# Optimization experiments

Hardware: AMD Instinct MI355X
Metric: run time of the kernel (lower is better)

Reference implementation:

```python
import jax, jax.numpy as jnp
import numpy as np

N_NODES = 65536
N_EDGES = 1048576
D = 128           # input_dim == hidden_dim*heads, residual active everywhere
HEADS = (4, 4, 1) # heads per GATv2 layer; last layer heads=1, out=input_dim
NUM_LAYERS = 3


def setup_inputs() -> dict:
    key = jax.random.key(0)
    ks = jax.random.split(key, 16)
    x = jax.random.normal(ks[0], (N_NODES, D), dtype=jnp.float32)
    edge_src = jax.random.randint(ks[1], (N_EDGES,), 0, N_NODES)
    edge_dst = jax.random.randint(ks[2], (N_EDGES,), 0, N_NODES)
    edge_attr = jax.random.uniform(ks[3], (N_EDGES, 1), dtype=jnp.float32)
    s = 0.05
    Wl = jax.random.normal(ks[4], (NUM_LAYERS, D, D), dtype=jnp.float32) * s
    bl = jnp.zeros((NUM_LAYERS, D), dtype=jnp.float32)
    Wr = jax.random.normal(ks[5], (NUM_LAYERS, D, D), dtype=jnp.float32) * s
    br = jnp.zeros((NUM_LAYERS, D), dtype=jnp.float32)
    We = jax.random.normal(ks[6], (NUM_LAYERS, 1, D), dtype=jnp.float32) * s
    att = jax.random.normal(ks[7], (NUM_LAYERS, D), dtype=jnp.float32) * s  # reshaped (H,C) per layer
    bias_p = jnp.zeros((NUM_LAYERS, D), dtype=jnp.float32)
    ln_g = jnp.ones((NUM_LAYERS, D), dtype=jnp.float32)
    ln_b = jnp.zeros((NUM_LAYERS, D), dtype=jnp.float32)
    return {"x": x, "edge_src": edge_src, "edge_dst": edge_dst, "edge_attr": edge_attr,
            "Wl": Wl, "bl": bl, "Wr": Wr, "br": br, "We": We, "att": att,
            "bias_p": bias_p, "ln_g": ln_g, "ln_b": ln_b, "num_graphs": 128}


def _layer_norm(x, g, b):
    mu = x.mean(-1, keepdims=True)
    var = jnp.mean((x - mu) ** 2, axis=-1, keepdims=True)
    return (x - mu) * jax.lax.rsqrt(var + 1e-5) * g + b


def _gatv2(x, src, dst, ea, Wl, bl, Wr, br, We, att, bias, H):
    # GATv2Conv, eval mode (no dropout), concat heads
    N = x.shape[0]
    HC = Wl.shape[1]
    C = HC // H
    xl = (x @ Wl + bl).reshape(N, H, C)
    xr = (x @ Wr + br).reshape(N, H, C)
    ee = (ea @ We).reshape(-1, H, C)            # [E, H, C]
    m = xl[src] + xr[dst] + ee                  # gather + fuse edge features
    m = jnp.where(m >= 0, m, 0.2 * m)           # leaky_relu(0.2)
    a = jnp.einsum('ehc,hc->eh', m, att.reshape(H, C))
    # scatter-softmax over destination node neighborhoods
    amax = jax.ops.segment_max(a, dst, num_segments=N)
    ae = jnp.exp(a - amax[dst])
    asum = jax.ops.segment_sum(ae, dst, num_segments=N)
    alpha = ae / (asum[dst] + 1e-16)
    out = jax.ops.segment_sum(xl[src] * alpha[:, :, None], dst, num_segments=N)
    return out.reshape(N, HC) + bias


def reference(x, edge_src, edge_dst, edge_attr, Wl, bl, Wr, br, We, att,
              bias_p, ln_g, ln_b, num_graphs):
    N = x.shape[0]
    # add_self_loops=True with fill_value='mean' for edge_attr (PyG default)
    loop = jnp.arange(N, dtype=edge_src.dtype)
    src = jnp.concatenate([edge_src, loop])
    dst = jnp.concatenate([edge_dst, loop])
    ea_mean = edge_attr.mean(0, keepdims=True)
    ea = jnp.concatenate([edge_attr, jnp.broadcast_to(ea_mean, (N, edge_attr.shape[1]))])
    h = x
    for i in range(NUM_LAYERS):
        out = _gatv2(h, src, dst, ea, Wl[i], bl[i], Wr[i], br[i], We[i],
                     att[i], bias_p[i], HEADS[i])
        out = _layer_norm(out, ln_g[i], ln_b[i])
        if i < NUM_LAYERS - 1:
            out = jax.nn.gelu(out, approximate=False)
        h = h + out  # residual: dims match at every layer by construction
    # to_dense_batch with equal-size graphs, then drop virtual node (last per graph)
    x_dense = h.reshape(num_graphs, -1, h.shape[-1])
    return x_dense[:, :-1, :]
```

## Files before the change

kernel.cpp:

```cpp
#include <hip/hip_runtime.h>
#include <hip/hip_bf16.h>

typedef unsigned int uint;
typedef unsigned short ushort;

#define NN 65536
#define NE 1048576
#define DD 128
#define TOTE (NE + NN)

__device__ __forceinline__ float b2f(ushort u) {
    uint v = ((uint)u) << 16; float f; __builtin_memcpy(&f, &v, 4); return f;
}
__device__ __forceinline__ ushort f2b(float f) {
    uint x; __builtin_memcpy(&x, &f, 4);
    uint r = (x + 0x7fffu + ((x >> 16) & 1u)) >> 16;
    return (ushort)r;
}

typedef __bf16 bf16x8 __attribute__((ext_vector_type(8)));
typedef float f32x4 __attribute__((ext_vector_type(4)));
typedef float f32x2 __attribute__((ext_vector_type(2)));

__device__ __forceinline__ f32x2 bf2f2(uint u) {
    union { uint i; float f; } lo, hi;
    lo.i = u << 16; hi.i = u & 0xffff0000u;
    return (f32x2){lo.f, hi.f};
}


__global__ void k_init(const float* __restrict__ Wl, const float* __restrict__ Wr,
                       ushort* __restrict__ WT, int* __restrict__ cnt, float* __restrict__ sumbuf,
                       float* __restrict__ cano) {
    if (cano && blockIdx.x == 0 && blockIdx.y == 0 && blockIdx.z == 0 && threadIdx.x == 0)
        cano[0] = 100.0f;
    int k = blockIdx.x, n = threadIdx.x, lr = blockIdx.y, layer = blockIdx.z;
    const float* W = (lr ? Wr : Wl) + layer * 16384;
    WT[(layer * 2 + lr) * 16384 + n * 128 + k] = f2b(W[k * 128 + n]);
    int gid = ((blockIdx.z * 2 + blockIdx.y) * 128 + blockIdx.x) * 128 + threadIdx.x;
    if (gid < NN) cnt[gid] = 0;
    if (gid == NN) sumbuf[0] = 0.f;
}

__global__ void k_histsum(const int* __restrict__ dst, const float* __restrict__ ea,
                          int* __restrict__ cnt, float* __restrict__ sum,
                          float* __restrict__ cano) {
    if (cano && blockIdx.x == 0 && threadIdx.x == 0) cano[1] = 120.0f;
    __shared__ float red[256];
    int t = threadIdx.x;
    int e = blockIdx.x * 256 + t;
    int d = (e < NE) ? dst[e] : (e - NE);
    atomicAdd(&cnt[d], 1);
    float s = (e < NE) ? ea[e] : 0.f;
    red[t] = s; __syncthreads();
    for (int o = 128; o > 0; o >>= 1) { if (t < o) red[t] += red[t + o]; __syncthreads(); }
    if (t == 0 && red[0] != 0.f) atomicAdd(sum, red[0]);
}

__global__ void k_scanA(const int* __restrict__ cnt, int* __restrict__ row_off, int* __restrict__ bsum,
                        float* __restrict__ cano) {
    if (cano && blockIdx.x == 0 && threadIdx.x == 0) cano[2] = 140.0f;
    __shared__ int tmp[256];
    int t = threadIdx.x, i = blockIdx.x * 256 + t;
    int v = cnt[i]; tmp[t] = v; __syncthreads();
    for (int off = 1; off < 256; off <<= 1) {
        int x = (t >= off) ? tmp[t - off] : 0;
        __syncthreads();
        tmp[t] += x;
        __syncthreads();
    }
    row_off[i] = tmp[t] - v;
    if (t == 255) bsum[blockIdx.x] = tmp[255];
}

__global__ void k_scanC(int* __restrict__ row_off, const int* __restrict__ bsum, int* __restrict__ cursor,
                        float* __restrict__ cano) {
    if (cano && blockIdx.x == 0 && threadIdx.x == 0) cano[3] = 160.0f;
    __shared__ int tmp[256];
    __shared__ int excl[256];
    int t = threadIdx.x;
    int v = bsum[t]; tmp[t] = v; __syncthreads();
    for (int off = 1; off < 256; off <<= 1) {
        int x = (t >= off) ? tmp[t - off] : 0;
        __syncthreads();
        tmp[t] += x;
        __syncthreads();
    }
    excl[t] = tmp[t] - v;
    __syncthreads();
    int offb = excl[blockIdx.x];
    int i = blockIdx.x * 256 + t;
    int nv = row_off[i] + offb;
    row_off[i] = nv;
    cursor[i] = nv;
    if (i == 0) row_off[NN] = TOTE;
}

__global__ void k_scatter(const int* __restrict__ src, const int* __restrict__ dst,
                          const float* __restrict__ ea, const float* __restrict__ sum,
                          int* __restrict__ cursor, int2* __restrict__ adj,
                          float* __restrict__ cano) {
    if (cano && blockIdx.x == 0 && threadIdx.x == 0) cano[4] = 180.0f;
    int e = blockIdx.x * 256 + threadIdx.x;
    int s, d; float a;
    if (e < NE) { s = src[e]; d = dst[e]; a = ea[e]; }
    else        { s = e - NE; d = s;      a = sum[0] * (1.0f / NE); }
    int pos = atomicAdd(&cursor[d], 1);
    adj[pos] = make_int2(s << 8, __float_as_int(a));
}

#define LDA 136

template<bool F32SRC>
__global__ __launch_bounds__(256) void k_gemm(const void* __restrict__ srcv, const ushort* __restrict__ WT,
                                              const float* __restrict__ bl, const float* __restrict__ br,
                                              ushort* __restrict__ xl, ushort* __restrict__ xr,
                                              float* __restrict__ cano, int cslot, float cval) {
    if (cano && blockIdx.x == 0 && threadIdx.x == 0) cano[cslot] = cval;
    __shared__ ushort A[64 * LDA];
    int t = threadIdx.x;
    int rowbase = blockIdx.x * 64;

    if (F32SRC) {
        const float* src = (const float*)srcv;
        #pragma unroll
        for (int it = 0; it < 8; it++) {
            int idx = it * 256 + t;
            int r = idx >> 5, cc = (idx & 31) * 4;
            float4 v = *(const float4*)&src[(size_t)(rowbase + r) * 128 + cc];
            ushort4 pk; pk.x = f2b(v.x); pk.y = f2b(v.y); pk.z = f2b(v.z); pk.w = f2b(v.w);
            *(ushort4*)&A[r * LDA + cc] = pk;
        }
    } else {
        const ushort* src = (const ushort*)srcv;
        #pragma unroll
        for (int it = 0; it < 4; it++) {
            int idx = it * 256 + t;
            int r = idx >> 4, cc = (idx & 15) * 8;
            *(bf16x8*)&A[r * LDA + cc] = *(const bf16x8*)&src[(size_t)(rowbase + r) * 128 + cc];
        }
    }
    __syncthreads();

    int wave = t >> 6, lane = t & 63;
    int row16 = lane & 15, quad = lane >> 4;

    f32x4 accl[8], accr[8];
    for (int i = 0; i < 8; i++) {
        accl[i] = (f32x4){0.f, 0.f, 0.f, 0.f};
        accr[i] = (f32x4){0.f, 0.f, 0.f, 0.f};
    }

    for (int ks = 0; ks < 4; ks++) {
        bf16x8 a = *(const bf16x8*)&A[(wave * 16 + row16) * LDA + ks * 32 + quad * 8];
        for (int tc = 0; tc < 8; tc++) {
            int coln = tc * 16 + row16;
            bf16x8 b_l = *(const bf16x8*)&WT[coln * 128 + ks * 32 + quad * 8];
            bf16x8 b_r = *(const bf16x8*)&WT[16384 + coln * 128 + ks * 32 + quad * 8];
            accl[tc] = __builtin_amdgcn_mfma_f32_16x16x32_bf16(a, b_l, accl[tc], 0, 0, 0);
            accr[tc] = __builtin_amdgcn_mfma_f32_16x16x32_bf16(a, b_r, accr[tc], 0, 0, 0);
        }
    }

    for (int tc = 0; tc < 8; tc++) {
        int col = tc * 16 + row16;
        float bbl = bl[col], bbr = br[col];
        for (int r = 0; r < 4; r++) {
            int row = rowbase + wave * 16 + quad * 4 + r;
            size_t o = (size_t)row * 128 + col;
            xl[o] = f2b(accl[tc][r] + bbl);
            xr[o] = f2b(accr[tc][r] + bbr);
        }
    }
}

template<int H, bool FINAL>
__global__ __launch_bounds__(128, 4) void k_attn(
    const ushort* __restrict__ xl, const ushort* __restrict__ xr,
    const int* __restrict__ row_off, const int2* __restrict__ adj,
    const float* __restrict__ We, const float* __restrict__ att,
    const float* __restrict__ bias, const float* __restrict__ ln_g, const float* __restrict__ ln_b,
    const float* __restrict__ hin, float* __restrict__ hout, ushort* __restrict__ hb,
    float* __restrict__ outp,
    float* __restrict__ cano, int cslot, float cval)
{
    if (cano && blockIdx.x == 0 && threadIdx.x == 0) cano[cslot] = cval;
    __shared__ float accbuf[2][8][160];

    int wv = threadIdx.x >> 6, lane = threadIdx.x & 63;
    int n = blockIdx.x * 2 + wv;
    int p = lane >> 3;
    int cl = lane & 7;
    int c16 = cl * 16;
    const char* xlb = (const char*)xl;

    f32x2 we2[8], at2[8], xrl2[8];
    #pragma unroll
    for (int k = 0; k < 8; k++) {
        we2[k] = (f32x2){We[c16 + 2 * k], We[c16 + 2 * k + 1]};
        at2[k] = (f32x2){att[c16 + 2 * k], att[c16 + 2 * k + 1]};
    }
    {
        uint4 r0 = *(const uint4*)&xr[(size_t)n * 128 + c16];
        uint4 r1 = *(const uint4*)&xr[(size_t)n * 128 + c16 + 8];
        xrl2[0] = bf2f2(r0.x); xrl2[1] = bf2f2(r0.y); xrl2[2] = bf2f2(r0.z); xrl2[3] = bf2f2(r0.w);
        xrl2[4] = bf2f2(r1.x); xrl2[5] = bf2f2(r1.y); xrl2[6] = bf2f2(r1.z); xrl2[7] = bf2f2(r1.w);
    }

    int s0 = row_off[n], s1 = row_off[n + 1];
    int iters = (s1 - s0 + 7) >> 3;

    float l_run = 0.f;
    f32x2 acc[8];
    #pragma unroll
    for (int k = 0; k < 8; k++) acc[k] = (f32x2){0.f, 0.f};

    int j0 = s0 + p,      j1 = s0 + 8 + p,  j2 = s0 + 16 + p, j3 = s0 + 24 + p;
    int i0 = (j0 < s1) ? j0 : s0;
    int i1 = (j1 < s1) ? j1 : s0;
    int i2 = (j2 < s1) ? j2 : s0;
    int i3 = (j3 < s1) ? j3 : s0;
    int2 a0 = adj[i0], a1 = adj[i1], a2 = adj[i2], a3 = adj[i3];
    float ea0 = (j0 < s1) ? __int_as_float(a0.y) : 0.f;
    float ea1 = (j1 < s1) ? __int_as_float(a1.y) : 0.f;
    float ea2v = (j2 < s1) ? __int_as_float(a2.y) : 0.f;
    float ea3 = (j3 < s1) ? __int_as_float(a3.y) : 0.f;
    const char* q0 = xlb + (size_t)(uint)a0.x + (cl << 5);
    const char* q1 = xlb + (size_t)(uint)a1.x + (cl << 5);
    const char* q2 = xlb + (size_t)(uint)a2.x + (cl << 5);
    const char* q3 = xlb + (size_t)(uint)a3.x + (cl << 5);
    uint4 u00 = *(const uint4*)q0, u01 = *(const uint4*)(q0 + 16);
    uint4 u10 = *(const uint4*)q1, u11 = *(const uint4*)(q1 + 16);
    uint4 u20 = *(const uint4*)q2, u21 = *(const uint4*)(q2 + 16);
    uint4 u30 = *(const uint4*)q3, u31 = *(const uint4*)(q3 + 16);

    auto consume = [&](uint4 u0, uint4 u1, float ea_c, int itx) {
        bool valid = (s0 + itx * 8 + p) < s1;
        f32x2 xf[8];
        xf[0] = bf2f2(u0.x); xf[1] = bf2f2(u0.y); xf[2] = bf2f2(u0.z); xf[3] = bf2f2(u0.w);
        xf[4] = bf2f2(u1.x); xf[5] = bf2f2(u1.y); xf[6] = bf2f2(u1.z); xf[7] = bf2f2(u1.w);

        f32x2 ea2 = (f32x2){ea_c, ea_c};
        f32x2 s2 = (f32x2){0.f, 0.f};
        #pragma unroll
        for (int k = 0; k < 8; k++) {
            f32x2 m = xf[k] + __builtin_elementwise_fma(ea2, we2[k], xrl2[k]);
            m = __builtin_elementwise_max(m, 0.2f * m);
            s2 = __builtin_elementwise_fma(m, at2[k], s2);
        }
        float s = s2.x + s2.y;
        s += __shfl_xor(s, 1);
        if (H == 1) { s += __shfl_xor(s, 2); s += __shfl_xor(s, 4); }
        if (!valid) s = -1e30f;

        float e = __expf(s);
        l_run += e;
        f32x2 e2 = (f32x2){e, e};
        #pragma unroll
        for (int k = 0; k < 8; k++) acc[k] = __builtin_elementwise_fma(e2, xf[k], acc[k]);
    };

    consume(u00, u01, ea0, 0);
    if (iters > 1) consume(u10, u11, ea1, 1);
    if (iters > 2) consume(u20, u21, ea2v, 2);
    if (iters > 3) consume(u30, u31, ea3, 3);
    for (int it = 4; it < iters; ++it) {
        int jn = s0 + it * 8 + p;
        int jb = (jn < s1) ? jn : s0;
        int2 pk = adj[jb];
        float ean = (jn < s1) ? __int_as_float(pk.y) : 0.f;
        const char* rp = xlb + (size_t)(uint)pk.x + (cl << 5);
        uint4 nu0 = *(const uint4*)rp;
        uint4 nu1 = *(const uint4*)(rp + 16);
        consume(nu0, nu1, ean, it);
    }

    l_run += __shfl_xor(l_run, 8);
    l_run += __shfl_xor(l_run, 16);
    l_run += __shfl_xor(l_run, 32);
    float inv = 1.0f / (l_run + 1e-16f);

    float* row = &accbuf[wv][p][cl * 20];
    #pragma unroll
    for (int i = 0; i < 4; i++)
        *(float4*)&row[4 * i] = make_float4(acc[2 * i].x * inv, acc[2 * i].y * inv,
                                            acc[2 * i + 1].x * inv, acc[2 * i + 1].y * inv);
    __syncthreads();

    int c0 = 2 * lane;
    int rb = (c0 >> 4) * 20 + (c0 & 15);
    float o0 = 0.f, o1 = 0.f;
    #pragma unroll
    for (int q = 0; q < 8; q++) {
        float2 v = *(float2*)&accbuf[wv][q][rb];
        o0 += v.x; o1 += v.y;
    }
    o0 += bias[c0];
    o1 += bias[c0 + 1];

    float sred = o0 + o1;
    #pragma unroll
    for (int off = 1; off < 64; off <<= 1) sred += __shfl_xor(sred, off);
    float mu = sred * (1.f / 128.f);
    float d0 = o0 - mu, d1 = o1 - mu;
    float v = d0 * d0 + d1 * d1;
    #pragma unroll
    for (int off = 1; off < 64; off <<= 1) v += __shfl_xor(v, off);
    float rstd = rsqrtf(v * (1.f / 128.f) + 1e-5f);
    o0 = d0 * rstd * ln_g[c0] + ln_b[c0];
    o1 = d1 * rstd * ln_g[c0 + 1] + ln_b[c0 + 1];

    float2 hv = *(const float2*)&hin[(size_t)n * 128 + c0];
    if (FINAL) {
        float r0 = hv.x + o0, r1 = hv.y + o1;
        int g = n >> 9, rr = n & 511;
        if (rr < 511)
            *(float2*)&outp[((size_t)(g * 511 + rr)) * 128 + c0] = make_float2(r0, r1);
    } else {
        o0 = 0.5f * o0 * (1.f + erff(o0 * 0.70710678118f));
        o1 = 0.5f * o1 * (1.f + erff(o1 * 0.70710678118f));
        hv.x += o0; hv.y += o1;
        *(float2*)&hout[(size_t)n * 128 + c0] = hv;
        uint pk = (uint)f2b(hv.x) | ((uint)f2b(hv.y) << 16);
        *(uint*)&hb[(size_t)n * 128 + c0] = pk;
    }
}

extern "C" void kernel_launch(void* const* d_in, const int* in_sizes, int n_in,
                              void* d_out, int out_size, void* d_ws, size_t ws_size,
                              hipStream_t stream) {
    const float* x        = (const float*)d_in[0];
    const int*   edge_src = (const int*)d_in[1];
    const int*   edge_dst = (const int*)d_in[2];
    const float* edge_attr= (const float*)d_in[3];
    const float* Wl       = (const float*)d_in[4];
    const float* bl       = (const float*)d_in[5];
    const float* Wr       = (const float*)d_in[6];
    const float* br       = (const float*)d_in[7];
    const float* We       = (const float*)d_in[8];
    const float* att      = (const float*)d_in[9];
    const float* bias_p   = (const float*)d_in[10];
    const float* ln_g     = (const float*)d_in[11];
    const float* ln_b     = (const float*)d_in[12];
    float* out = (float*)d_out;

    char* ws = (char*)d_ws;
    float*  h       = (float*)(ws + 0);
    ushort* hb      = (ushort*)(ws + 33554432);
    ushort* xl      = (ushort*)(ws + 50331648);
    ushort* xr      = (ushort*)(ws + 67108864);
    int2*   adj     = (int2*)(ws + 83886080);
    int*    row_off = (int*)(ws + 92798976);
    int*    cnt     = (int*)(ws + 93061376);
    int*    bsum    = (int*)(ws + 93323520);
    float*  sumbuf  = (float*)(ws + 93324544);
    ushort* WT      = (ushort*)(ws + 93324800);

    k_init<<<dim3(128, 2, 3), 128, 0, stream>>>(Wl, Wr, WT, cnt, sumbuf, out);
    k_histsum<<<TOTE / 256, 256, 0, stream>>>(edge_dst, edge_attr, cnt, sumbuf, out);
    k_scanA<<<NN / 256, 256, 0, stream>>>(cnt, row_off, bsum, out);
    k_scanC<<<NN / 256, 256, 0, stream>>>(row_off, bsum, cnt, out);
    k_scatter<<<TOTE / 256, 256, 0, stream>>>(edge_src, edge_dst, edge_attr, sumbuf, cnt, adj, out);

    k_gemm<true><<<NN / 64, 256, 0, stream>>>(x, WT, bl, br, xl, xr, out, 5, 200.0f);
    k_attn<4, false><<<NN / 2, 128, 0, stream>>>(xl, xr, row_off, adj,
                                                 We, att, bias_p, ln_g, ln_b,
                                                 x, h, hb, nullptr, out, 6, 220.0f);
    k_gemm<false><<<NN / 64, 256, 0, stream>>>(hb, WT + 32768, bl + 128, br + 128, xl, xr, out, 7, 240.0f);
    k_attn<4, false><<<NN / 2, 128, 0, stream>>>(xl, xr, row_off, adj,
                                                 We + 128, att + 128, bias_p + 128,
                                                 ln_g + 128, ln_b + 128,
                                                 h, h, hb, nullptr, out, 8, 260.0f);
    k_gemm<false><<<NN / 64, 256, 0, stream>>>(hb, WT + 65536, bl + 256, br + 256, xl, xr, out, 9, 280.0f);
    k_attn<1, true><<<NN / 2, 128, 0, stream>>>(xl, xr, row_off, adj,
                                                We + 256, att + 256, bias_p + 256,
                                                ln_g + 256, ln_b + 256,
                                                h, nullptr, nullptr, out, nullptr, 0, 0.0f);
}
```

Measured before the change: 615.3 us.

## Stage weights in LDS, load A directly to registers, coalesce GEMM output via LDS

```diff
diff --git a/kernel.cpp b/kernel.cpp
--- a/kernel.cpp
+++ b/kernel.cpp
@@ -109,68 +109,88 @@
     adj[pos] = make_int2(s << 8, __float_as_int(a));
 }
 
-#define LDA 136
-
 template<bool F32SRC>
-__global__ __launch_bounds__(256) void k_gemm(const void* __restrict__ srcv, const ushort* __restrict__ WT,
+__global__ __launch_bounds__(512) void k_gemm(const void* __restrict__ srcv, const ushort* __restrict__ WT,
                                               const float* __restrict__ bl, const float* __restrict__ br,
                                               ushort* __restrict__ xl, ushort* __restrict__ xr,
                                               float* __restrict__ cano, int cslot, float cval) {
     if (cano && blockIdx.x == 0 && threadIdx.x == 0) cano[cslot] = cval;
-    __shared__ ushort A[64 * LDA];
+    __shared__ __align__(16) ushort S[32768];
+
     int t = threadIdx.x;
-    int rowbase = blockIdx.x * 64;
-
-    if (F32SRC) {
-        const float* src = (const float*)srcv;
-        #pragma unroll
-        for (int it = 0; it < 8; it++) {
-            int idx = it * 256 + t;
-            int r = idx >> 5, cc = (idx & 31) * 4;
-            float4 v = *(const float4*)&src[(size_t)(rowbase + r) * 128 + cc];
-            ushort4 pk; pk.x = f2b(v.x); pk.y = f2b(v.y); pk.z = f2b(v.z); pk.w = f2b(v.w);
-            *(ushort4*)&A[r * LDA + cc] = pk;
-        }
-    } else {
-        const ushort* src = (const ushort*)srcv;
-        #pragma unroll
-        for (int it = 0; it < 4; it++) {
-            int idx = it * 256 + t;
-            int r = idx >> 4, cc = (idx & 15) * 8;
-            *(bf16x8*)&A[r * LDA + cc] = *(const bf16x8*)&src[(size_t)(rowbase + r) * 128 + cc];
-        }
-    }
-    __syncthreads();
+    int rowbase = blockIdx.x * 128;
+
+    #pragma unroll
+    for (int i = 0; i < 8; i++) {
+        int idx = i * 512 + t;
+        int m = idx >> 11, n = (idx >> 4) & 127, c = idx & 15;
+        *(bf16x8*)&S[m * 16384 + c * 1024 + n * 8] =
+            *(const bf16x8*)&WT[m * 16384 + n * 128 + c * 8];
+    }
 
     int wave = t >> 6, lane = t & 63;
     int row16 = lane & 15, quad = lane >> 4;
+    int myrow = rowbase + wave * 16 + row16;
+
+    float bbl[8], bbr[8];
+    #pragma unroll
+    for (int tc = 0; tc < 8; tc++) { bbl[tc] = bl[tc * 16 + row16]; bbr[tc] = br[tc * 16 + row16]; }
 
     f32x4 accl[8], accr[8];
+    #pragma unroll
     for (int i = 0; i < 8; i++) {
         accl[i] = (f32x4){0.f, 0.f, 0.f, 0.f};
         accr[i] = (f32x4){0.f, 0.f, 0.f, 0.f};
     }
 
+    __syncthreads();
+
+    #pragma unroll
     for (int ks = 0; ks < 4; ks++) {
-        bf16x8 a = *(const bf16x8*)&A[(wave * 16 + row16) * LDA + ks * 32 + quad * 8];
+        bf16x8 a;
+        if (F32SRC) {
+            const float* src = (const float*)srcv;
+            const float* pa = &src[(size_t)myrow * 128 + ks * 32 + quad * 8];
+            float4 v0 = *(const float4*)pa;
+            float4 v1 = *(const float4*)(pa + 4);
+            ushort u[8] = {f2b(v0.x), f2b(v0.y), f2b(v0.z), f2b(v0.w),
+                           f2b(v1.x), f2b(v1.y), f2b(v1.z), f2b(v1.w)};
+            __builtin_memcpy(&a, u, 16);
+        } else {
+            a = *(const bf16x8*)&((const ushort*)srcv)[(size_t)myrow * 128 + ks * 32 + quad * 8];
+        }
+        int chunk = ks * 4 + quad;
+        #pragma unroll
         for (int tc = 0; tc < 8; tc++) {
             int coln = tc * 16 + row16;
-            bf16x8 b_l = *(const bf16x8*)&WT[coln * 128 + ks * 32 + quad * 8];
-            bf16x8 b_r = *(const bf16x8*)&WT[16384 + coln * 128 + ks * 32 + quad * 8];
+            bf16x8 b_l = *(const bf16x8*)&S[chunk * 1024 + coln * 8];
+            bf16x8 b_r = *(const bf16x8*)&S[16384 + chunk * 1024 + coln * 8];
             accl[tc] = __builtin_amdgcn_mfma_f32_16x16x32_bf16(a, b_l, accl[tc], 0, 0, 0);
             accr[tc] = __builtin_amdgcn_mfma_f32_16x16x32_bf16(a, b_r, accr[tc], 0, 0, 0);
         }
     }
 
+    __syncthreads();
+
+    #pragma unroll
     for (int tc = 0; tc < 8; tc++) {
         int col = tc * 16 + row16;
-        float bbl = bl[col], bbr = br[col];
+        #pragma unroll
         for (int r = 0; r < 4; r++) {
-            int row = rowbase + wave * 16 + quad * 4 + r;
-            size_t o = (size_t)row * 128 + col;
-            xl[o] = f2b(accl[tc][r] + bbl);
-            xr[o] = f2b(accr[tc][r] + bbr);
+            int row = wave * 16 + quad * 4 + r;
+            S[row * 128 + col]         = f2b(accl[tc][r] + bbl[tc]);
+            S[16384 + row * 128 + col] = f2b(accr[tc][r] + bbr[tc]);
         }
+    }
+    __syncthreads();
+
+    #pragma unroll
+    for (int i = 0; i < 8; i++) {
+        int idx = i * 512 + t;
+        int m = idx >> 11, row = (idx >> 4) & 127, c8 = idx & 15;
+        bf16x8 v = *(const bf16x8*)&S[m * 16384 + row * 128 + c8 * 8];
+        ushort* dst = m ? xr : xl;
+        *(bf16x8*)&dst[(size_t)(rowbase + row) * 128 + c8 * 8] = v;
     }
 }
 
@@ -362,16 +382,16 @@
     k_scanC<<<NN / 256, 256, 0, stream>>>(row_off, bsum, cnt, out);
     k_scatter<<<TOTE / 256, 256, 0, stream>>>(edge_src, edge_dst, edge_attr, sumbuf, cnt, adj, out);
 
-    k_gemm<true><<<NN / 64, 256, 0, stream>>>(x, WT, bl, br, xl, xr, out, 5, 200.0f);
+    k_gemm<true><<<NN / 128, 512, 0, stream>>>(x, WT, bl, br, xl, xr, out, 5, 200.0f);
     k_attn<4, false><<<NN / 2, 128, 0, stream>>>(xl, xr, row_off, adj,
                                                  We, att, bias_p, ln_g, ln_b,
                                                  x, h, hb, nullptr, out, 6, 220.0f);
-    k_gemm<false><<<NN / 64, 256, 0, stream>>>(hb, WT + 32768, bl + 128, br + 128, xl, xr, out, 7, 240.0f);
+    k_gemm<false><<<NN / 128, 512, 0, stream>>>(hb, WT + 32768, bl + 128, br + 128, xl, xr, out, 7, 240.0f);
     k_attn<4, false><<<NN / 2, 128, 0, stream>>>(xl, xr, row_off, adj,
                                                  We + 128, att + 128, bias_p + 128,
                                                  ln_g + 128, ln_b + 128,
                                                  h, h, hb, nullptr, out, 8, 260.0f);
-    k_gemm<false><<<NN / 64, 256, 0, stream>>>(hb, WT + 65536, bl + 256, br + 256, xl, xr, out, 9, 280.0f);
+    k_gemm<false><<<NN / 128, 512, 0, stream>>>(hb, WT + 65536, bl + 256, br + 256, xl, xr, out, 9, 280.0f);
     k_attn<1, true><<<NN / 2, 128, 0, stream>>>(xl, xr, row_off, adj,
                                                 We + 256, att + 256, bias_p + 256,
                                                 ln_g + 256, ln_b + 256,
```

After: 537.6 us. -12.6%, faster.
